# Optimization experiments

Hardware: AMD Instinct MI355X
Metric: run time of the kernel (lower is better)

## Reference

```python
import jax, jax.numpy as jnp
import numpy as np

N_NODES = 100000
N_EDGES = 300000
D = 128
HID = 128

def setup_inputs() -> dict:
    key = jax.random.key(0)
    ks = jax.random.split(key, 12)
    s = lambda fan_in: 1.0 / np.sqrt(fan_in)
    return {
        "user_emb": jax.random.normal(ks[0], (N_NODES, D), jnp.float32),
        "item_emb": jax.random.normal(ks[1], (N_NODES, D), jnp.float32),
        "ei_ui": jax.random.randint(ks[2], (2, N_EDGES), 0, N_NODES, jnp.int64),
        "ei_iu": jax.random.randint(ks[3], (2, N_EDGES), 0, N_NODES, jnp.int64),
        "W_bi_ui": jax.random.normal(ks[4], (2 * D, HID), jnp.float32) * s(2 * D),
        "b_bi_ui": jnp.zeros((HID,), jnp.float32),
        "W1_ui": jax.random.normal(ks[5], (HID, HID), jnp.float32) * s(HID),
        "b1_ui": jnp.zeros((HID,), jnp.float32),
        "W2_ui": jax.random.normal(ks[6], (HID, 1), jnp.float32) * s(HID),
        "b2_ui": jnp.zeros((1,), jnp.float32),
        "W_bi_iu": jax.random.normal(ks[7], (2 * D, HID), jnp.float32) * s(2 * D),
        "b_bi_iu": jnp.zeros((HID,), jnp.float32),
        "W1_iu": jax.random.normal(ks[8], (HID, HID), jnp.float32) * s(HID),
        "b1_iu": jnp.zeros((HID,), jnp.float32),
        "W2_iu": jax.random.normal(ks[9], (HID, 1), jnp.float32) * s(HID),
        "b2_iu": jnp.zeros((1,), jnp.float32),
    }

def _decode_edge_type(src_emb, dst_emb, edge_index, W_bi, b_bi, W1, b1, W2, b2):
    # gather endpoint embeddings and concat -> [E, 2D]
    e = jnp.concatenate([src_emb[edge_index[0]], dst_emb[edge_index[1]]], axis=1)
    h = jax.nn.elu(e @ W_bi + b_bi)          # bilinear -> ELU
    h = jax.nn.elu(h @ W1 + b1)              # linear1 -> ELU
    p = jax.nn.sigmoid(h @ W2 + b2)          # linear2 -> sigmoid
    return p.reshape(-1)                     # [E]

def reference(user_emb, item_emb, ei_ui, ei_iu,
              W_bi_ui, b_bi_ui, W1_ui, b1_ui, W2_ui, b2_ui,
              W_bi_iu, b_bi_iu, W1_iu, b1_iu, W2_iu, b2_iu):
    # edge type (user, clicks, item): source=user, target=item
    p_ui = _decode_edge_type(user_emb, item_emb, ei_ui,
                             W_bi_ui, b_bi_ui, W1_ui, b1_ui, W2_ui, b2_ui)
    # edge type (item, clicked_by, user): source=item, target=user
    p_iu = _decode_edge_type(item_emb, user_emb, ei_iu,
                             W_bi_iu, b_bi_iu, W1_iu, b1_iu, W2_iu, b2_iu)
    return jnp.stack([p_ui, p_iu])  # [2, E]
```

## Files before the change

kernel.cpp:

```cpp
#include <hip/hip_runtime.h>

typedef __attribute__((ext_vector_type(8))) short short8;
typedef __attribute__((ext_vector_type(4))) float float4v;
typedef __attribute__((ext_vector_type(4))) int int4v;

#define E_EDGES 300000
#define EPB 64
#define NBLK ((E_EDGES + EPB - 1) / EPB)

__device__ __forceinline__ short f2bf(float f) {
    unsigned u = __float_as_uint(f);
    return (short)((u + 0x7FFFu + ((u >> 16) & 1u)) >> 16);
}
__device__ __forceinline__ unsigned pk_bf16(float a, float b) {
    unsigned ua = __float_as_uint(a), ub = __float_as_uint(b);
    ua += 0x7FFFu + ((ua >> 16) & 1u);
    ub += 0x7FFFu + ((ub >> 16) & 1u);
    return __builtin_amdgcn_perm(ub, ua, 0x07060302);
}

__device__ __forceinline__ void cp16(const void* g, void* l) {
    __builtin_amdgcn_global_load_lds(
        (const __attribute__((address_space(1))) unsigned int*)g,
        (__attribute__((address_space(3))) unsigned int*)l, 16, 0, 0);
}

__global__ void prep_weights(const float* __restrict__ Wbi_ui, const float* __restrict__ W1_ui,
                             const float* __restrict__ Wbi_iu, const float* __restrict__ W1_iu,
                             short* __restrict__ ws) {
    __shared__ short tr[64 * 68];
    const int t = blockIdx.y;
    const int m = blockIdx.x;
    const float* W; int k0, n0, obase;
    if (m < 8) {
        int kt = m >> 1, nh = m & 1;
        W = t ? Wbi_iu : Wbi_ui; k0 = kt * 64; n0 = nh * 64;
        obase = t * 32768 + kt * 8192;
    } else {
        int mm = m - 8; int kt = mm >> 1, nh = mm & 1;
        W = t ? W1_iu : W1_ui; k0 = kt * 64; n0 = nh * 64;
        obase = 65536 + t * 16384 + kt * 8192;
    }
    const int tid = threadIdx.x;
    for (int it = 0; it < 16; ++it) {
        int flat = it * 256 + tid;
        int kk = flat >> 6, nn = flat & 63;
        tr[nn * 68 + kk] = f2bf(W[(size_t)(k0 + kk) * 128 + n0 + nn]);
    }
    __syncthreads();
    for (int it = 0; it < 16; ++it) {
        int flat = it * 256 + tid;
        int nn = flat >> 6, kk = flat & 63;
        int n = n0 + nn;
        ws[obase + n * 64 + (kk ^ ((n & 7) << 3))] = tr[nn * 68 + kk];
    }
}

__launch_bounds__(256, 4)
__global__ void edge_decoder(
    const float* __restrict__ user_emb, const float* __restrict__ item_emb,
    const int* __restrict__ ei_ui, const int* __restrict__ ei_iu,
    const float* __restrict__ b_bi_ui, const float* __restrict__ b1_ui,
    const float* __restrict__ W2_ui, const float* __restrict__ b2_ui,
    const float* __restrict__ b_bi_iu, const float* __restrict__ b1_iu,
    const float* __restrict__ W2_iu, const float* __restrict__ b2_iu,
    const short* __restrict__ ws, float* __restrict__ out)
{
    __shared__ short Blds[128 * 64];
    __shared__ short Hlds[4 * 16 * 136];

    const int type = blockIdx.y;
    const int e0 = blockIdx.x * EPB;
    const int tid = threadIdx.x;
    const int wave = tid >> 6, lane = tid & 63;
    const int q = lane >> 4, ln = lane & 15;

    const float* srcT = type ? item_emb : user_emb;
    const float* dstT = type ? user_emb : item_emb;
    const int*   ei   = type ? ei_iu : ei_ui;
    const float* bbi  = type ? b_bi_iu : b_bi_ui;
    const float* b1v  = type ? b1_iu : b1_ui;
    const float* W2v  = type ? W2_iu : W2_ui;
    const float* b2v  = type ? b2_iu : b2_ui;
    const short* WbiT = ws + type * 32768;
    const short* W1T  = ws + 65536 + type * 16384;

    const int erow = e0 + wave * 16 + ln;
    const int safe = (erow < E_EDGES) ? erow : 0;
    const int si = ei[safe];
    const int di = ei[E_EDGES + safe];

    for (int c = 0; c < 4; ++c)
        cp16(WbiT + c * 2048 + tid * 8, Blds + c * 2048 + tid * 8);

    short8 a[8];
    for (int ks = 0; ks < 8; ++ks) {
        const float* p = (ks < 4) ? (srcT + (size_t)si * 128 + ks * 32 + q * 8)
                                  : (dstT + (size_t)di * 128 + (ks - 4) * 32 + q * 8);
        float4v v0 = ((const float4v*)p)[0];
        float4v v1 = ((const float4v*)p)[1];
        int4v w = { (int)pk_bf16(v0[0], v0[1]), (int)pk_bf16(v0[2], v0[3]),
                    (int)pk_bf16(v1[0], v1[1]), (int)pk_bf16(v1[2], v1[3]) };
        a[ks] = *(short8*)&w;
    }

    float4v acc[8];
    for (int nt = 0; nt < 8; ++nt) acc[nt] = (float4v){0.f, 0.f, 0.f, 0.f};

    const int swz = (ln & 7) << 3;

    for (int kt = 0; kt < 4; ++kt) {
        __syncthreads();
        for (int ks2 = 0; ks2 < 2; ++ks2) {
            int ka = (ks2 * 32 + q * 8) ^ swz;
            for (int nt = 0; nt < 8; ++nt) {
                short8 bf = *(const short8*)&Blds[(nt * 16 + ln) * 64 + ka];
                acc[nt] = __builtin_amdgcn_mfma_f32_16x16x32_bf16(a[kt * 2 + ks2], bf, acc[nt], 0, 0, 0);
            }
        }
        __syncthreads();
        const short* nxt = (kt < 3) ? (WbiT + (kt + 1) * 8192) : W1T;
        for (int c = 0; c < 4; ++c)
            cp16(nxt + c * 2048 + tid * 8, Blds + c * 2048 + tid * 8);
    }

    short* Hw = Hlds + wave * (16 * 136);
    for (int nt = 0; nt < 8; ++nt) {
        int col = nt * 16 + ln;
        float bb = bbi[col];
        float4v v = acc[nt];
        for (int r = 0; r < 4; ++r) {
            float x = v[r] + bb;
            float h = x > 0.f ? x : (__expf(x) - 1.f);
            Hw[(q * 4 + r) * 136 + col] = f2bf(h);
        }
    }
    short8 a2[4];
    for (int ks = 0; ks < 4; ++ks)
        a2[ks] = *(const short8*)&Hw[ln * 136 + ks * 32 + q * 8];

    for (int nt = 0; nt < 8; ++nt) acc[nt] = (float4v){0.f, 0.f, 0.f, 0.f};

    for (int kt = 0; kt < 2; ++kt) {
        __syncthreads();
        for (int ks2 = 0; ks2 < 2; ++ks2) {
            int ka = (ks2 * 32 + q * 8) ^ swz;
            for (int nt = 0; nt < 8; ++nt) {
                short8 bf = *(const short8*)&Blds[(nt * 16 + ln) * 64 + ka];
                acc[nt] = __builtin_amdgcn_mfma_f32_16x16x32_bf16(a2[kt * 2 + ks2], bf, acc[nt], 0, 0, 0);
            }
        }
        __syncthreads();
        if (kt == 0)
            for (int c = 0; c < 4; ++c)
                cp16(W1T + 8192 + c * 2048 + tid * 8, Blds + c * 2048 + tid * 8);
    }

    float s0 = 0.f, s1 = 0.f, s2 = 0.f, s3 = 0.f;
    for (int nt = 0; nt < 8; ++nt) {
        int col = nt * 16 + ln;
        float bb = b1v[col], wv = W2v[col];
        float4v v = acc[nt];
        float x;
        x = v[0] + bb; x = x > 0.f ? x : (__expf(x) - 1.f); s0 += x * wv;
        x = v[1] + bb; x = x > 0.f ? x : (__expf(x) - 1.f); s1 += x * wv;
        x = v[2] + bb; x = x > 0.f ? x : (__expf(x) - 1.f); s2 += x * wv;
        x = v[3] + bb; x = x > 0.f ? x : (__expf(x) - 1.f); s3 += x * wv;
    }
    for (int off = 1; off < 16; off <<= 1) {
        s0 += __shfl_xor(s0, off);
        s1 += __shfl_xor(s1, off);
        s2 += __shfl_xor(s2, off);
        s3 += __shfl_xor(s3, off);
    }
    if (ln < 4) {
        float sv = (ln == 0) ? s0 : (ln == 1) ? s1 : (ln == 2) ? s2 : s3;
        int e = e0 + wave * 16 + q * 4 + ln;
        if (e < E_EDGES) {
            float z = sv + b2v[0];
            out[type * E_EDGES + e] = 1.f / (1.f + __expf(-z));
        }
    }
}

extern "C" void kernel_launch(void* const* d_in, const int* in_sizes, int n_in,
                              void* d_out, int out_size, void* d_ws, size_t ws_size,
                              hipStream_t stream) {
    const float* user_emb = (const float*)d_in[0];
    const float* item_emb = (const float*)d_in[1];
    const int*   ei_ui    = (const int*)d_in[2];
    const int*   ei_iu    = (const int*)d_in[3];
    const float* W_bi_ui  = (const float*)d_in[4];
    const float* b_bi_ui  = (const float*)d_in[5];
    const float* W1_ui    = (const float*)d_in[6];
    const float* b1_ui    = (const float*)d_in[7];
    const float* W2_ui    = (const float*)d_in[8];
    const float* b2_ui    = (const float*)d_in[9];
    const float* W_bi_iu  = (const float*)d_in[10];
    const float* b_bi_iu  = (const float*)d_in[11];
    const float* W1_iu    = (const float*)d_in[12];
    const float* b1_iu    = (const float*)d_in[13];
    const float* W2_iu    = (const float*)d_in[14];
    const float* b2_iu    = (const float*)d_in[15];
    short* ws  = (short*)d_ws;
    float* out = (float*)d_out;

    hipLaunchKernelGGL(prep_weights, dim3(12, 2), dim3(256), 0, stream,
                       W_bi_ui, W1_ui, W_bi_iu, W1_iu, ws);
    hipLaunchKernelGGL(edge_decoder, dim3(NBLK, 2), dim3(256), 0, stream,
                       user_emb, item_emb, ei_ui, ei_iu,
                       b_bi_ui, b1_ui, W2_ui, b2_ui,
                       b_bi_iu, b1_iu, W2_iu, b2_iu,
                       ws, out);
}
```

Measured before the change: 270.9 us.

## Switch to 32x32x16 MFMA with swapped operands and 128 edges per block

```diff
diff --git a/kernel.cpp b/kernel.cpp
--- a/kernel.cpp
+++ b/kernel.cpp
@@ -1,11 +1,13 @@
 #include <hip/hip_runtime.h>
 
 typedef __attribute__((ext_vector_type(8))) short short8;
+typedef __attribute__((ext_vector_type(16))) float float16v;
 typedef __attribute__((ext_vector_type(4))) float float4v;
+typedef __attribute__((ext_vector_type(2))) int int2v;
 typedef __attribute__((ext_vector_type(4))) int int4v;
 
 #define E_EDGES 300000
-#define EPB 64
+#define EPB 128
 #define NBLK ((E_EDGES + EPB - 1) / EPB)
 
 __device__ __forceinline__ short f2bf(float f) {
@@ -56,7 +58,7 @@
     }
 }
 
-__launch_bounds__(256, 4)
+__launch_bounds__(256, 3)
 __global__ void edge_decoder(
     const float* __restrict__ user_emb, const float* __restrict__ item_emb,
     const int* __restrict__ ei_ui, const int* __restrict__ ei_iu,
@@ -67,13 +69,14 @@
     const short* __restrict__ ws, float* __restrict__ out)
 {
     __shared__ short Blds[128 * 64];
-    __shared__ short Hlds[4 * 16 * 136];
+    __shared__ short Hlds[4 * 32 * 136];
+    __shared__ float bbis[128], b1s[128], w2s[128];
 
     const int type = blockIdx.y;
     const int e0 = blockIdx.x * EPB;
     const int tid = threadIdx.x;
     const int wave = tid >> 6, lane = tid & 63;
-    const int q = lane >> 4, ln = lane & 15;
+    const int q2 = lane >> 5, ln = lane & 31;
 
     const float* srcT = type ? item_emb : user_emb;
     const float* dstT = type ? user_emb : item_emb;
@@ -85,37 +88,40 @@
     const short* WbiT = ws + type * 32768;
     const short* W1T  = ws + 65536 + type * 16384;
 
-    const int erow = e0 + wave * 16 + ln;
+    const int erow = e0 + wave * 32 + ln;
     const int safe = (erow < E_EDGES) ? erow : 0;
     const int si = ei[safe];
     const int di = ei[E_EDGES + safe];
 
+    if (tid < 128) { bbis[tid] = bbi[tid]; b1s[tid] = b1v[tid]; w2s[tid] = W2v[tid]; }
+
     for (int c = 0; c < 4; ++c)
         cp16(WbiT + c * 2048 + tid * 8, Blds + c * 2048 + tid * 8);
 
-    short8 a[8];
-    for (int ks = 0; ks < 8; ++ks) {
-        const float* p = (ks < 4) ? (srcT + (size_t)si * 128 + ks * 32 + q * 8)
-                                  : (dstT + (size_t)di * 128 + (ks - 4) * 32 + q * 8);
+    short8 eb[16];
+    for (int ks = 0; ks < 16; ++ks) {
+        const float* p = (ks < 8) ? (srcT + (size_t)si * 128 + ks * 16 + q2 * 8)
+                                  : (dstT + (size_t)di * 128 + (ks - 8) * 16 + q2 * 8);
         float4v v0 = ((const float4v*)p)[0];
         float4v v1 = ((const float4v*)p)[1];
         int4v w = { (int)pk_bf16(v0[0], v0[1]), (int)pk_bf16(v0[2], v0[3]),
                     (int)pk_bf16(v1[0], v1[1]), (int)pk_bf16(v1[2], v1[3]) };
-        a[ks] = *(short8*)&w;
-    }
-
-    float4v acc[8];
-    for (int nt = 0; nt < 8; ++nt) acc[nt] = (float4v){0.f, 0.f, 0.f, 0.f};
-
-    const int swz = (ln & 7) << 3;
+        eb[ks] = *(short8*)&w;
+    }
+
+    float16v acc[4];
+    for (int mt = 0; mt < 4; ++mt)
+        for (int i = 0; i < 16; ++i) acc[mt][i] = 0.f;
+
+    const int swz = ln & 7;
 
     for (int kt = 0; kt < 4; ++kt) {
         __syncthreads();
-        for (int ks2 = 0; ks2 < 2; ++ks2) {
-            int ka = (ks2 * 32 + q * 8) ^ swz;
-            for (int nt = 0; nt < 8; ++nt) {
-                short8 bf = *(const short8*)&Blds[(nt * 16 + ln) * 64 + ka];
-                acc[nt] = __builtin_amdgcn_mfma_f32_16x16x32_bf16(a[kt * 2 + ks2], bf, acc[nt], 0, 0, 0);
+        for (int ks = 0; ks < 4; ++ks) {
+            int koff = ((ks * 2 + q2) ^ swz) * 8;
+            for (int mt = 0; mt < 4; ++mt) {
+                short8 af = *(const short8*)&Blds[(mt * 32 + ln) * 64 + koff];
+                acc[mt] = __builtin_amdgcn_mfma_f32_32x32x16_bf16(af, eb[kt * 4 + ks], acc[mt], 0, 0, 0);
             }
         }
         __syncthreads();
@@ -124,30 +130,33 @@
             cp16(nxt + c * 2048 + tid * 8, Blds + c * 2048 + tid * 8);
     }
 
-    short* Hw = Hlds + wave * (16 * 136);
-    for (int nt = 0; nt < 8; ++nt) {
-        int col = nt * 16 + ln;
-        float bb = bbi[col];
-        float4v v = acc[nt];
-        for (int r = 0; r < 4; ++r) {
-            float x = v[r] + bb;
-            float h = x > 0.f ? x : (__expf(x) - 1.f);
-            Hw[(q * 4 + r) * 136 + col] = f2bf(h);
-        }
-    }
-    short8 a2[4];
-    for (int ks = 0; ks < 4; ++ks)
-        a2[ks] = *(const short8*)&Hw[ln * 136 + ks * 32 + q * 8];
-
-    for (int nt = 0; nt < 8; ++nt) acc[nt] = (float4v){0.f, 0.f, 0.f, 0.f};
+    short* Hw = Hlds + wave * (32 * 136);
+    for (int mt = 0; mt < 4; ++mt) {
+        for (int g = 0; g < 4; ++g) {
+            int h0 = mt * 32 + g * 8 + q2 * 4;
+            float4v bb = *(const float4v*)&bbis[h0];
+            float x0 = acc[mt][g * 4 + 0] + bb[0]; x0 = x0 > 0.f ? x0 : (__expf(x0) - 1.f);
+            float x1 = acc[mt][g * 4 + 1] + bb[1]; x1 = x1 > 0.f ? x1 : (__expf(x1) - 1.f);
+            float x2 = acc[mt][g * 4 + 2] + bb[2]; x2 = x2 > 0.f ? x2 : (__expf(x2) - 1.f);
+            float x3 = acc[mt][g * 4 + 3] + bb[3]; x3 = x3 > 0.f ? x3 : (__expf(x3) - 1.f);
+            int2v pw = { (int)pk_bf16(x0, x1), (int)pk_bf16(x2, x3) };
+            *(int2v*)&Hw[ln * 136 + h0] = pw;
+        }
+    }
+    short8 h2[8];
+    for (int ks = 0; ks < 8; ++ks)
+        h2[ks] = *(const short8*)&Hw[ln * 136 + ks * 16 + q2 * 8];
+
+    for (int mt = 0; mt < 4; ++mt)
+        for (int i = 0; i < 16; ++i) acc[mt][i] = 0.f;
 
     for (int kt = 0; kt < 2; ++kt) {
         __syncthreads();
-        for (int ks2 = 0; ks2 < 2; ++ks2) {
-            int ka = (ks2 * 32 + q * 8) ^ swz;
-            for (int nt = 0; nt < 8; ++nt) {
-                short8 bf = *(const short8*)&Blds[(nt * 16 + ln) * 64 + ka];
-                acc[nt] = __builtin_amdgcn_mfma_f32_16x16x32_bf16(a2[kt * 2 + ks2], bf, acc[nt], 0, 0, 0);
+        for (int ks = 0; ks < 4; ++ks) {
+            int koff = ((ks * 2 + q2) ^ swz) * 8;
+            for (int mt = 0; mt < 4; ++mt) {
+                short8 af = *(const short8*)&Blds[(mt * 32 + ln) * 64 + koff];
+                acc[mt] = __builtin_amdgcn_mfma_f32_32x32x16_bf16(af, h2[kt * 4 + ks], acc[mt], 0, 0, 0);
             }
         }
         __syncthreads();
@@ -156,28 +165,24 @@
                 cp16(W1T + 8192 + c * 2048 + tid * 8, Blds + c * 2048 + tid * 8);
     }
 
-    float s0 = 0.f, s1 = 0.f, s2 = 0.f, s3 = 0.f;
-    for (int nt = 0; nt < 8; ++nt) {
-        int col = nt * 16 + ln;
-        float bb = b1v[col], wv = W2v[col];
-        float4v v = acc[nt];
-        float x;
-        x = v[0] + bb; x = x > 0.f ? x : (__expf(x) - 1.f); s0 += x * wv;
-        x = v[1] + bb; x = x > 0.f ? x : (__expf(x) - 1.f); s1 += x * wv;
-        x = v[2] + bb; x = x > 0.f ? x : (__expf(x) - 1.f); s2 += x * wv;
-        x = v[3] + bb; x = x > 0.f ? x : (__expf(x) - 1.f); s3 += x * wv;
-    }
-    for (int off = 1; off < 16; off <<= 1) {
-        s0 += __shfl_xor(s0, off);
-        s1 += __shfl_xor(s1, off);
-        s2 += __shfl_xor(s2, off);
-        s3 += __shfl_xor(s3, off);
-    }
-    if (ln < 4) {
-        float sv = (ln == 0) ? s0 : (ln == 1) ? s1 : (ln == 2) ? s2 : s3;
-        int e = e0 + wave * 16 + q * 4 + ln;
+    float s = 0.f;
+    for (int mt = 0; mt < 4; ++mt) {
+        for (int g = 0; g < 4; ++g) {
+            int h0 = mt * 32 + g * 8 + q2 * 4;
+            float4v bb = *(const float4v*)&b1s[h0];
+            float4v wv = *(const float4v*)&w2s[h0];
+            for (int r = 0; r < 4; ++r) {
+                float x = acc[mt][g * 4 + r] + bb[r];
+                x = x > 0.f ? x : (__expf(x) - 1.f);
+                s += x * wv[r];
+            }
+        }
+    }
+    s += __shfl_xor(s, 32);
+    if (lane < 32) {
+        int e = e0 + wave * 32 + ln;
         if (e < E_EDGES) {
-            float z = sv + b2v[0];
+            float z = s + b2v[0];
             out[type * E_EDGES + e] = 1.f / (1.f + __expf(-z));
         }
     }
```

Result: slower. 283.1 us (+4.5%).
